# Kernel tuning notes

Measured on AMD Instinct MI355X. Metric: run time of the kernel, lower is better.

Reference implementation:

```python
import jax, jax.numpy as jnp
import numpy as np

EPS = 1e-5
B, C, H, W = 64, 256, 64, 64


def _masked_mean(p9, r0, r1, c0, c1):
    # p9: [B,3,3,9,H,W]; r0,r1: [B,3] int row bounds (per i); c0,c1: [B,3] int col bounds (per j)
    Hh, Ww = p9.shape[-2], p9.shape[-1]
    rows = jnp.arange(Hh, dtype=jnp.int32)
    cols = jnp.arange(Ww, dtype=jnp.int32)
    mr = (rows[None, None, :] >= r0[..., None]) & (rows[None, None, :] < r1[..., None])  # [B,3,H]
    mc = (cols[None, None, :] >= c0[..., None]) & (cols[None, None, :] < c1[..., None])  # [B,3,W]
    mask = (mr[:, :, None, :, None] & mc[:, None, :, None, :]).astype(p9.dtype)  # [B,3,3,H,W]
    cnt = mask.sum((-2, -1))  # [B,3,3]
    s = jnp.einsum('bijkhw,bijhw->bijk', p9, mask)
    return jnp.where(cnt[..., None] > 0, s / jnp.maximum(cnt, 1.0)[..., None], 0.0)  # [B,3,3,9]


def _subj_obj_bounds(bbox, Hh, Ww):
    # bbox: [B,4] = [y0,y1,x0,x1] normalized
    y0, y1, x0, x1 = bbox[:, 0], bbox[:, 1], bbox[:, 2], bbox[:, 3]
    ch = (y1 - y0) / 3.0
    cw = (x1 - x0) / 3.0
    idx = jnp.arange(3, dtype=bbox.dtype)
    r0 = jnp.floor(Hh * (y0[:, None] + idx * ch[:, None])).astype(jnp.int32)
    r1 = jnp.floor(Hh * (y0[:, None] + (idx + 1.0) * ch[:, None])).astype(jnp.int32)
    dr = r1 <= r0
    r1n = jnp.where(dr & (r1 < Hh - 1), r1 + 1, r1)
    r0n = jnp.where(dr & (r1 >= Hh - 1), r0 - 1, r0)
    c0 = jnp.floor(Ww * (x0[:, None] + idx * cw[:, None])).astype(jnp.int32)
    c1 = jnp.floor(Ww * (x0[:, None] + (idx + 1.0) * cw[:, None])).astype(jnp.int32)
    dc = c1 <= c0
    c1n = jnp.where(dc & (c1 < Ww), c1 + 1, c1)
    c0n = jnp.where(dc & (c1 >= Ww), c0 - 1, c0)
    return r0n, r1n, c0n, c1n


def _joint_bounds(bbox, bbox_s, bbox_o, Hh, Ww):
    # intersection of bbox with the 3x3 cells of union(bbox_s, bbox_o)
    uy0 = jnp.minimum(bbox_s[:, 0], bbox_o[:, 0])
    uy1 = jnp.maximum(bbox_s[:, 1], bbox_o[:, 1])
    ux0 = jnp.minimum(bbox_s[:, 2], bbox_o[:, 2])
    ux1 = jnp.maximum(bbox_s[:, 3], bbox_o[:, 3])
    ch = (uy1 - uy0) / 3.0
    cw = (ux1 - ux0) / 3.0
    idx = jnp.arange(3, dtype=bbox.dtype)
    ylo = uy0[:, None] + idx * ch[:, None]
    yhi = uy0[:, None] + (idx + 1.0) * ch[:, None]
    xlo = ux0[:, None] + idx * cw[:, None]
    xhi = ux0[:, None] + (idx + 1.0) * cw[:, None]
    r0 = jnp.floor(Hh * jnp.maximum(bbox[:, 0][:, None], ylo)).astype(jnp.int32)
    r1 = jnp.floor(Hh * jnp.minimum(bbox[:, 1][:, None], yhi)).astype(jnp.int32)
    c0 = jnp.floor(Ww * jnp.maximum(bbox[:, 2][:, None], xlo)).astype(jnp.int32)
    c1 = jnp.floor(Ww * jnp.minimum(bbox[:, 3][:, None], xhi)).astype(jnp.int32)
    return r0, r1, c0, c1


def setup_inputs() -> dict:
    key = jax.random.key(0)
    ks = jax.random.split(key, 16)
    feat = jax.random.normal(ks[0], (B, C, H, W), dtype=jnp.float32)

    def make_bbox(k):
        k1, k2, k3, k4 = jax.random.split(k, 4)
        y0 = jax.random.uniform(k1, (B,), minval=0.0, maxval=0.4)
        y1 = jnp.minimum(y0 + jax.random.uniform(k2, (B,), minval=0.3, maxval=0.55), 0.99)
        x0 = jax.random.uniform(k3, (B,), minval=0.0, maxval=0.4)
        x1 = jnp.minimum(x0 + jax.random.uniform(k4, (B,), minval=0.3, maxval=0.55), 0.99)
        return jnp.stack([y0, y1, x0, x1], axis=1).astype(jnp.float32)

    bbox_s = make_bbox(ks[1])
    bbox_o = make_bbox(ks[2])
    predicate = jax.random.uniform(ks[3], (B, 9), dtype=jnp.float32)
    conv_w = jax.random.normal(ks[4], (324, 256), dtype=jnp.float32) * 0.02
    conv_b = jax.random.normal(ks[5], (324,), dtype=jnp.float32) * 0.02
    bn2_g = jax.random.uniform(ks[6], (324,), minval=0.5, maxval=1.5)
    bn2_b = jax.random.normal(ks[7], (324,)) * 0.02
    bn2_m = jax.random.normal(ks[8], (324,)) * 0.02
    bn2_v = jax.random.uniform(ks[9], (324,), minval=0.5, maxval=1.5)
    fc1_w = jax.random.normal(ks[10], (40, 81), dtype=jnp.float32) * 0.1
    fc1_b = jnp.zeros((40,), jnp.float32)
    bn1_g = jax.random.uniform(ks[11], (40,), minval=0.5, maxval=1.5)
    bn1_b = jax.random.normal(ks[12], (40,)) * 0.02
    bn1_m = jax.random.normal(ks[13], (40,)) * 0.02
    bn1_v = jax.random.uniform(ks[14], (40,), minval=0.5, maxval=1.5)
    fc2_w = jax.random.normal(ks[15], (9, 40), dtype=jnp.float32) * 0.1
    fc2_b = jnp.zeros((9,), jnp.float32)
    return dict(feat=feat, bbox_s=bbox_s, bbox_o=bbox_o, predicate=predicate,
                conv_w=conv_w, conv_b=conv_b, bn2_g=bn2_g, bn2_b=bn2_b, bn2_m=bn2_m, bn2_v=bn2_v,
                fc1_w=fc1_w, fc1_b=fc1_b, bn1_g=bn1_g, bn1_b=bn1_b, bn1_m=bn1_m, bn1_v=bn1_v,
                fc2_w=fc2_w, fc2_b=fc2_b)


def reference(feat, bbox_s, bbox_o, predicate, conv_w, conv_b, bn2_g, bn2_b, bn2_m, bn2_v,
              fc1_w, fc1_b, bn1_g, bn1_b, bn1_m, bn1_v, fc2_w, fc2_b):
    # 1x1 conv 256 -> 324, then BatchNorm2d (inference mode)
    prs = jnp.einsum('bchw,oc->bohw', feat, conv_w) + conv_b[None, :, None, None]
    prs = (prs - bn2_m[None, :, None, None]) * (bn2_g / jnp.sqrt(bn2_v + EPS))[None, :, None, None] + bn2_b[None, :, None, None]
    Bb, _, Hh, Ww = prs.shape
    # channel layout: start = i*27 + j*9 + k  ->  reshape to [B,3,3,9,H,W]
    def bank(lo):
        return prs[:, lo:lo + 81].reshape(Bb, 3, 3, 9, Hh, Ww)
    prs_s, prs_o, prs_js, prs_jo = bank(0), bank(81), bank(162), bank(243)

    feature_s = _masked_mean(prs_s, *_subj_obj_bounds(bbox_s, Hh, Ww))
    feature_o = _masked_mean(prs_o, *_subj_obj_bounds(bbox_o, Hh, Ww))
    feature_j = (_masked_mean(prs_js, *_joint_bounds(bbox_s, bbox_s, bbox_o, Hh, Ww)) +
                 _masked_mean(prs_jo, *_joint_bounds(bbox_o, bbox_s, bbox_o, Hh, Ww)))

    f = feature_s + feature_o + feature_j            # [B,3,3,9]
    f = jnp.transpose(f, (0, 3, 1, 2)).reshape(Bb, 81)  # torch layout [B,9,3,3] flattened

    h = f @ fc1_w.T + fc1_b
    h = (h - bn1_m) * (bn1_g / jnp.sqrt(bn1_v + EPS)) + bn1_b
    logits = h @ fc2_w.T + fc2_b
    return jnp.sum(logits * predicate, axis=1)
```

## Files before the change

kernel.cpp:

```cpp
#include <hip/hip_runtime.h>
#include <hip/hip_bf16.h>
#include <cstdint>

#define BB 64
#define CC 256
#define HH 64
#define WW 64
#define EPSF 1e-5f

__device__ __forceinline__ void subj_bounds_dev(float y0, float y1, float x0, float x1,
                                                int* dst ) {
    float ch = __fdiv_rn(__fsub_rn(y1, y0), 3.0f);
    float cw = __fdiv_rn(__fsub_rn(x1, x0), 3.0f);
    for (int i = 0; i < 3; ++i) {
        float fi = (float)i;
        int R0 = (int)floorf(__fmul_rn((float)HH, __fadd_rn(y0, __fmul_rn(fi, ch))));
        int R1 = (int)floorf(__fmul_rn((float)HH, __fadd_rn(y0, __fmul_rn(__fadd_rn(fi, 1.0f), ch))));
        bool dr = (R1 <= R0);
        int R1n = (dr && (R1 < HH - 1)) ? R1 + 1 : R1;
        int R0n = (dr && (R1 >= HH - 1)) ? R0 - 1 : R0;
        int C0 = (int)floorf(__fmul_rn((float)WW, __fadd_rn(x0, __fmul_rn(fi, cw))));
        int C1 = (int)floorf(__fmul_rn((float)WW, __fadd_rn(x0, __fmul_rn(__fadd_rn(fi, 1.0f), cw))));
        bool dc = (C1 <= C0);
        int C1n = (dc && (C1 < WW)) ? C1 + 1 : C1;
        int C0n = (dc && (C1 >= WW)) ? C0 - 1 : C0;
        dst[i]     = R0n;
        dst[3 + i] = R1n;
        dst[6 + i] = C0n;
        dst[9 + i] = C1n;
    }
}

__device__ __forceinline__ void joint_bounds_dev(float uy0, float uy1, float ux0, float ux1,
                                                 float by0, float by1, float bx0, float bx1,
                                                 int* dst ) {
    float ch = __fdiv_rn(__fsub_rn(uy1, uy0), 3.0f);
    float cw = __fdiv_rn(__fsub_rn(ux1, ux0), 3.0f);
    for (int i = 0; i < 3; ++i) {
        float fi = (float)i;
        float ylo = __fadd_rn(uy0, __fmul_rn(fi, ch));
        float yhi = __fadd_rn(uy0, __fmul_rn(__fadd_rn(fi, 1.0f), ch));
        float xlo = __fadd_rn(ux0, __fmul_rn(fi, cw));
        float xhi = __fadd_rn(ux0, __fmul_rn(__fadd_rn(fi, 1.0f), cw));
        dst[i]     = (int)floorf(__fmul_rn((float)HH, fmaxf(by0, ylo)));
        dst[3 + i] = (int)floorf(__fmul_rn((float)HH, fminf(by1, yhi)));
        dst[6 + i] = (int)floorf(__fmul_rn((float)WW, fmaxf(bx0, xlo)));
        dst[9 + i] = (int)floorf(__fmul_rn((float)WW, fminf(bx1, xhi)));
    }
}

__global__ void k_bounds(const float* __restrict__ bbox_s,
                         const float* __restrict__ bbox_o,
                         int* __restrict__ bnds,
                         float* __restrict__ cntf) {
    int b = blockIdx.x * blockDim.x + threadIdx.x;
    if (b >= BB) return;
    float sy0 = bbox_s[b * 4 + 0], sy1 = bbox_s[b * 4 + 1];
    float sx0 = bbox_s[b * 4 + 2], sx1 = bbox_s[b * 4 + 3];
    float oy0 = bbox_o[b * 4 + 0], oy1 = bbox_o[b * 4 + 1];
    float ox0 = bbox_o[b * 4 + 2], ox1 = bbox_o[b * 4 + 3];

    int loc[4][12];
    subj_bounds_dev(sy0, sy1, sx0, sx1, loc[0]);
    subj_bounds_dev(oy0, oy1, ox0, ox1, loc[1]);
    float uy0 = fminf(sy0, oy0), uy1 = fmaxf(sy1, oy1);
    float ux0 = fminf(sx0, ox0), ux1 = fmaxf(sx1, ox1);
    joint_bounds_dev(uy0, uy1, ux0, ux1, sy0, sy1, sx0, sx1, loc[2]);
    joint_bounds_dev(uy0, uy1, ux0, ux1, oy0, oy1, ox0, ox1, loc[3]);

    int* ob = bnds + b * 48;
    float* oc = cntf + b * 36;
    for (int bank = 0; bank < 4; ++bank) {
        for (int q = 0; q < 12; ++q) ob[bank * 12 + q] = loc[bank][q];
        for (int i = 0; i < 3; ++i) {
            int rl = max(loc[bank][i], 0);
            int rh = min(loc[bank][3 + i], HH);
            int nrows = max(0, rh - rl);
            for (int j = 0; j < 3; ++j) {
                int cl = max(loc[bank][6 + j], 0);
                int chh = min(loc[bank][9 + j], WW);
                int ncols = max(0, chh - cl);
                oc[bank * 9 + i * 3 + j] = (float)(nrows * ncols);
            }
        }
    }
}

__global__ __launch_bounds__(64) void k_region_sums(const float* __restrict__ feat,
                                                    const int* __restrict__ bnds,
                                                    float* __restrict__ M) {
    int b = blockIdx.x >> 8;
    int c = blockIdx.x & 255;
    int l = threadIdx.x;

    __shared__ float S[64 * 65];

    const float4* src = (const float4*)(feat + ((size_t)(b * CC + c)) * (HH * WW));
    for (int it = 0; it < 16; ++it) {
        int f = it * 256 + l * 4;
        int h = f >> 6, w = f & 63;
        float4 v = src[it * 64 + l];
        float* dst = &S[h * 65 + w];
        dst[0] = v.x; dst[1] = v.y; dst[2] = v.z; dst[3] = v.w;
    }
    __syncthreads();

    {
        float run = 0.0f;
        int base = l * 65;
        for (int i = 0; i < 64; ++i) { run += S[base + i]; S[base + i] = run; }
    }
    __syncthreads();

    {
        float run = 0.0f;
        for (int i = 0; i < 64; ++i) { run += S[i * 65 + l]; S[i * 65 + l] = run; }
    }
    __syncthreads();

    if (l < 36) {
        const int* bk = bnds + b * 48 + (l / 9) * 12;
        int ij = l % 9, i = ij / 3, j = ij % 3;
        int r0 = bk[i], r1 = bk[3 + i], c0 = bk[6 + j], c1 = bk[9 + j];
        int rl = max(r0, 0), rh = min(r1, HH);
        int cl = max(c0, 0), chh = min(c1, WW);
        float s = 0.0f;
        if (rh > rl && chh > cl) {
            float a = S[(rh - 1) * 65 + (chh - 1)];
            float q = (cl > 0) ? S[(rh - 1) * 65 + (cl - 1)] : 0.0f;
            float p = (rl > 0) ? S[(rl - 1) * 65 + (chh - 1)] : 0.0f;
            float d = (rl > 0 && cl > 0) ? S[(rl - 1) * 65 + (cl - 1)] : 0.0f;
            s = a - q - p + d;
        }
        M[((size_t)(b * CC + c)) * 36 + l] = s;
    }
}

__global__ __launch_bounds__(384) void k_head(const float* __restrict__ M,
                                              const float* __restrict__ cntf,
                                              const float* __restrict__ conv_w,
                                              const float* __restrict__ conv_b,
                                              const float* __restrict__ g2,
                                              const float* __restrict__ b2,
                                              const float* __restrict__ m2,
                                              const float* __restrict__ v2,
                                              const float* __restrict__ fc1_w,
                                              const float* __restrict__ fc1_b,
                                              const float* __restrict__ g1,
                                              const float* __restrict__ b1,
                                              const float* __restrict__ m1,
                                              const float* __restrict__ v1,
                                              const float* __restrict__ fc2_w,
                                              const float* __restrict__ fc2_b,
                                              const float* __restrict__ pred,
                                              float* __restrict__ out) {
    int b = blockIdx.x;
    int t = threadIdx.x;

    __shared__ float Ml[256 * 37];
    __shared__ float val[324];
    __shared__ float fv[81];
    __shared__ float hv[40];
    __shared__ float lg[9];

    for (int i = t; i < 256 * 36; i += 384) {
        int c = i / 36, r = i - c * 36;
        Ml[c * 37 + r] = M[(size_t)b * (256 * 36) + i];
    }
    __syncthreads();

    if (t < 324) {
        int region = t / 9, k = t - region * 9;
        int bank = region / 9, ij = region - bank * 9;
        int ii = ij / 3, jj = ij % 3;
        int o = bank * 81 + ii * 27 + jj * 9 + k;
        float cnt = cntf[b * 36 + region];
        float v = 0.0f;
        if (cnt > 0.0f) {
            const float* w = conv_w + o * 256;
            float dot = 0.0f;
            #pragma unroll 8
            for (int c = 0; c < 256; ++c) dot += w[c] * Ml[c * 37 + region];
            float mean = dot / cnt;
            float sc = g2[o] / sqrtf(v2[o] + EPSF);
            v = (mean + conv_b[o] - m2[o]) * sc + b2[o];
        }
        val[region * 9 + k] = v;
    }
    __syncthreads();

    if (t < 81) {
        int k = t / 9, ij = t - k * 9;
        fv[t] = val[(0 + ij) * 9 + k] + val[(9 + ij) * 9 + k] +
                val[(18 + ij) * 9 + k] + val[(27 + ij) * 9 + k];
    }
    __syncthreads();

    if (t < 40) {
        float h = fc1_b[t];
        for (int u = 0; u < 81; ++u) h += fv[u] * fc1_w[t * 81 + u];
        h = (h - m1[t]) * (g1[t] / sqrtf(v1[t] + EPSF)) + b1[t];
        hv[t] = h;
    }
    __syncthreads();

    if (t < 9) {
        float lgt = fc2_b[t];
        for (int u = 0; u < 40; ++u) lgt += hv[u] * fc2_w[t * 40 + u];
        lg[t] = lgt * pred[b * 9 + t];
    }
    __syncthreads();

    if (t == 0) {
        float s = 0.0f;
        for (int i = 0; i < 9; ++i) s += lg[i];
        out[b] = s;
    }
}

extern "C" void kernel_launch(void* const* d_in, const int* in_sizes, int n_in,
                              void* d_out, int out_size, void* d_ws, size_t ws_size,
                              hipStream_t stream) {
    const float* feat   = (const float*)d_in[0];
    const float* bbox_s = (const float*)d_in[1];
    const float* bbox_o = (const float*)d_in[2];
    const float* pred   = (const float*)d_in[3];
    const float* conv_w = (const float*)d_in[4];
    const float* conv_b = (const float*)d_in[5];
    const float* g2     = (const float*)d_in[6];
    const float* b2     = (const float*)d_in[7];
    const float* m2     = (const float*)d_in[8];
    const float* v2     = (const float*)d_in[9];
    const float* fc1_w  = (const float*)d_in[10];
    const float* fc1_b  = (const float*)d_in[11];
    const float* g1     = (const float*)d_in[12];
    const float* b1     = (const float*)d_in[13];
    const float* m1     = (const float*)d_in[14];
    const float* v1     = (const float*)d_in[15];
    const float* fc2_w  = (const float*)d_in[16];
    const float* fc2_b  = (const float*)d_in[17];
    float* out = (float*)d_out;

    char* ws = (char*)d_ws;
    int*   bnds = (int*)ws;
    float* cntf = (float*)(ws + 12288);
    float* M    = (float*)(ws + 32768);

    k_bounds<<<1, 64, 0, stream>>>(bbox_s, bbox_o, bnds, cntf);
    k_region_sums<<<BB * CC, 64, 0, stream>>>(feat, bnds, M);
    k_head<<<BB, 384, 0, stream>>>(M, cntf, conv_w, conv_b, g2, b2, m2, v2,
                                   fc1_w, fc1_b, g1, b1, m1, v1, fc2_w, fc2_b,
                                   pred, out);
}
```

Before: 63.28 us.

## Fuse bounds into region-sum kernel and software-pipeline four planes per block

Drops the separate bounds kernel. Region bounds and counts are now recomputed inline, in the region-sum kernel and in the head, which removes one launch and a dependency. Each region-sum block now handles four channel planes and prefetches the next plane into registers while scanning the current one. This hides global load latency, at the cost of many more registers per thread and four times fewer blocks.

```diff
diff --git a/kernel.cpp b/kernel.cpp
--- a/kernel.cpp
+++ b/kernel.cpp
@@ -4,140 +4,149 @@
 
 #define BB 64
 #define CC 256
-#define HH 64
-#define WW 64
 #define EPSF 1e-5f
-
-__device__ __forceinline__ void subj_bounds_dev(float y0, float y1, float x0, float x1,
-                                                int* dst ) {
-    float ch = __fdiv_rn(__fsub_rn(y1, y0), 3.0f);
-    float cw = __fdiv_rn(__fsub_rn(x1, x0), 3.0f);
-    for (int i = 0; i < 3; ++i) {
-        float fi = (float)i;
-        int R0 = (int)floorf(__fmul_rn((float)HH, __fadd_rn(y0, __fmul_rn(fi, ch))));
-        int R1 = (int)floorf(__fmul_rn((float)HH, __fadd_rn(y0, __fmul_rn(__fadd_rn(fi, 1.0f), ch))));
+#define PLANES 4
+
+__device__ __forceinline__ void region_bounds(int bank, int i, int j,
+                                              float sy0, float sy1, float sx0, float sx1,
+                                              float oy0, float oy1, float ox0, float ox1,
+                                              int& r0, int& r1, int& c0, int& c1) {
+    float fi = (float)i, fj = (float)j;
+    if (bank < 2) {
+        float y0 = bank ? oy0 : sy0, y1 = bank ? oy1 : sy1;
+        float x0 = bank ? ox0 : sx0, x1 = bank ? ox1 : sx1;
+        float ch = __fdiv_rn(__fsub_rn(y1, y0), 3.0f);
+        float cw = __fdiv_rn(__fsub_rn(x1, x0), 3.0f);
+        int R0 = (int)floorf(__fmul_rn(64.0f, __fadd_rn(y0, __fmul_rn(fi, ch))));
+        int R1 = (int)floorf(__fmul_rn(64.0f, __fadd_rn(y0, __fmul_rn(__fadd_rn(fi, 1.0f), ch))));
         bool dr = (R1 <= R0);
-        int R1n = (dr && (R1 < HH - 1)) ? R1 + 1 : R1;
-        int R0n = (dr && (R1 >= HH - 1)) ? R0 - 1 : R0;
-        int C0 = (int)floorf(__fmul_rn((float)WW, __fadd_rn(x0, __fmul_rn(fi, cw))));
-        int C1 = (int)floorf(__fmul_rn((float)WW, __fadd_rn(x0, __fmul_rn(__fadd_rn(fi, 1.0f), cw))));
+        r1 = (dr && (R1 < 63)) ? R1 + 1 : R1;
+        r0 = (dr && (R1 >= 63)) ? R0 - 1 : R0;
+        int C0 = (int)floorf(__fmul_rn(64.0f, __fadd_rn(x0, __fmul_rn(fj, cw))));
+        int C1 = (int)floorf(__fmul_rn(64.0f, __fadd_rn(x0, __fmul_rn(__fadd_rn(fj, 1.0f), cw))));
         bool dc = (C1 <= C0);
-        int C1n = (dc && (C1 < WW)) ? C1 + 1 : C1;
-        int C0n = (dc && (C1 >= WW)) ? C0 - 1 : C0;
-        dst[i]     = R0n;
-        dst[3 + i] = R1n;
-        dst[6 + i] = C0n;
-        dst[9 + i] = C1n;
-    }
-}
-
-__device__ __forceinline__ void joint_bounds_dev(float uy0, float uy1, float ux0, float ux1,
-                                                 float by0, float by1, float bx0, float bx1,
-                                                 int* dst ) {
-    float ch = __fdiv_rn(__fsub_rn(uy1, uy0), 3.0f);
-    float cw = __fdiv_rn(__fsub_rn(ux1, ux0), 3.0f);
-    for (int i = 0; i < 3; ++i) {
-        float fi = (float)i;
+        c1 = (dc && (C1 < 64)) ? C1 + 1 : C1;
+        c0 = (dc && (C1 >= 64)) ? C0 - 1 : C0;
+    } else {
+        float by0 = (bank == 2) ? sy0 : oy0, by1 = (bank == 2) ? sy1 : oy1;
+        float bx0 = (bank == 2) ? sx0 : ox0, bx1 = (bank == 2) ? sx1 : ox1;
+        float uy0 = fminf(sy0, oy0), uy1 = fmaxf(sy1, oy1);
+        float ux0 = fminf(sx0, ox0), ux1 = fmaxf(sx1, ox1);
+        float ch = __fdiv_rn(__fsub_rn(uy1, uy0), 3.0f);
+        float cw = __fdiv_rn(__fsub_rn(ux1, ux0), 3.0f);
         float ylo = __fadd_rn(uy0, __fmul_rn(fi, ch));
         float yhi = __fadd_rn(uy0, __fmul_rn(__fadd_rn(fi, 1.0f), ch));
-        float xlo = __fadd_rn(ux0, __fmul_rn(fi, cw));
-        float xhi = __fadd_rn(ux0, __fmul_rn(__fadd_rn(fi, 1.0f), cw));
-        dst[i]     = (int)floorf(__fmul_rn((float)HH, fmaxf(by0, ylo)));
-        dst[3 + i] = (int)floorf(__fmul_rn((float)HH, fminf(by1, yhi)));
-        dst[6 + i] = (int)floorf(__fmul_rn((float)WW, fmaxf(bx0, xlo)));
-        dst[9 + i] = (int)floorf(__fmul_rn((float)WW, fminf(bx1, xhi)));
-    }
-}
-
-__global__ void k_bounds(const float* __restrict__ bbox_s,
-                         const float* __restrict__ bbox_o,
-                         int* __restrict__ bnds,
-                         float* __restrict__ cntf) {
-    int b = blockIdx.x * blockDim.x + threadIdx.x;
-    if (b >= BB) return;
+        float xlo = __fadd_rn(ux0, __fmul_rn(fj, cw));
+        float xhi = __fadd_rn(ux0, __fmul_rn(__fadd_rn(fj, 1.0f), cw));
+        r0 = (int)floorf(__fmul_rn(64.0f, fmaxf(by0, ylo)));
+        r1 = (int)floorf(__fmul_rn(64.0f, fminf(by1, yhi)));
+        c0 = (int)floorf(__fmul_rn(64.0f, fmaxf(bx0, xlo)));
+        c1 = (int)floorf(__fmul_rn(64.0f, fminf(bx1, xhi)));
+    }
+}
+
+__global__ __launch_bounds__(64) void k_region_sums(const float* __restrict__ feat,
+                                                    const float* __restrict__ bbox_s,
+                                                    const float* __restrict__ bbox_o,
+                                                    float* __restrict__ M) {
+    int blk = blockIdx.x;
+    int l = threadIdx.x;
+    int pid0 = blk * PLANES;
+    int b = pid0 >> 8;
+
     float sy0 = bbox_s[b * 4 + 0], sy1 = bbox_s[b * 4 + 1];
     float sx0 = bbox_s[b * 4 + 2], sx1 = bbox_s[b * 4 + 3];
     float oy0 = bbox_o[b * 4 + 0], oy1 = bbox_o[b * 4 + 1];
     float ox0 = bbox_o[b * 4 + 2], ox1 = bbox_o[b * 4 + 3];
 
-    int loc[4][12];
-    subj_bounds_dev(sy0, sy1, sx0, sx1, loc[0]);
-    subj_bounds_dev(oy0, oy1, ox0, ox1, loc[1]);
-    float uy0 = fminf(sy0, oy0), uy1 = fmaxf(sy1, oy1);
-    float ux0 = fminf(sx0, ox0), ux1 = fmaxf(sx1, ox1);
-    joint_bounds_dev(uy0, uy1, ux0, ux1, sy0, sy1, sx0, sx1, loc[2]);
-    joint_bounds_dev(uy0, uy1, ux0, ux1, oy0, oy1, ox0, ox1, loc[3]);
-
-    int* ob = bnds + b * 48;
-    float* oc = cntf + b * 36;
-    for (int bank = 0; bank < 4; ++bank) {
-        for (int q = 0; q < 12; ++q) ob[bank * 12 + q] = loc[bank][q];
-        for (int i = 0; i < 3; ++i) {
-            int rl = max(loc[bank][i], 0);
-            int rh = min(loc[bank][3 + i], HH);
-            int nrows = max(0, rh - rl);
-            for (int j = 0; j < 3; ++j) {
-                int cl = max(loc[bank][6 + j], 0);
-                int chh = min(loc[bank][9 + j], WW);
-                int ncols = max(0, chh - cl);
-                oc[bank * 9 + i * 3 + j] = (float)(nrows * ncols);
-            }
-        }
-    }
-}
-
-__global__ __launch_bounds__(64) void k_region_sums(const float* __restrict__ feat,
-                                                    const int* __restrict__ bnds,
-                                                    float* __restrict__ M) {
-    int b = blockIdx.x >> 8;
-    int c = blockIdx.x & 255;
-    int l = threadIdx.x;
+    int rl = 0, rh = 0, cl = 0, chh = 0;
+    if (l < 36) {
+        int bank = l / 9, ij = l % 9, i = ij / 3, j = ij % 3;
+        int r0, r1, c0, c1;
+        region_bounds(bank, i, j, sy0, sy1, sx0, sx1, oy0, oy1, ox0, ox1, r0, r1, c0, c1);
+        rl = max(r0, 0); rh = min(r1, 64);
+        cl = max(c0, 0); chh = min(c1, 64);
+    }
 
     __shared__ float S[64 * 65];
-
-    const float4* src = (const float4*)(feat + ((size_t)(b * CC + c)) * (HH * WW));
-    for (int it = 0; it < 16; ++it) {
-        int f = it * 256 + l * 4;
-        int h = f >> 6, w = f & 63;
-        float4 v = src[it * 64 + l];
-        float* dst = &S[h * 65 + w];
-        dst[0] = v.x; dst[1] = v.y; dst[2] = v.z; dst[3] = v.w;
-    }
-    __syncthreads();
-
-    {
-        float run = 0.0f;
-        int base = l * 65;
-        for (int i = 0; i < 64; ++i) { run += S[base + i]; S[base + i] = run; }
-    }
-    __syncthreads();
-
-    {
-        float run = 0.0f;
-        for (int i = 0; i < 64; ++i) { run += S[i * 65 + l]; S[i * 65 + l] = run; }
-    }
-    __syncthreads();
-
-    if (l < 36) {
-        const int* bk = bnds + b * 48 + (l / 9) * 12;
-        int ij = l % 9, i = ij / 3, j = ij % 3;
-        int r0 = bk[i], r1 = bk[3 + i], c0 = bk[6 + j], c1 = bk[9 + j];
-        int rl = max(r0, 0), rh = min(r1, HH);
-        int cl = max(c0, 0), chh = min(c1, WW);
-        float s = 0.0f;
-        if (rh > rl && chh > cl) {
-            float a = S[(rh - 1) * 65 + (chh - 1)];
-            float q = (cl > 0) ? S[(rh - 1) * 65 + (cl - 1)] : 0.0f;
-            float p = (rl > 0) ? S[(rl - 1) * 65 + (chh - 1)] : 0.0f;
-            float d = (rl > 0 && cl > 0) ? S[(rl - 1) * 65 + (cl - 1)] : 0.0f;
-            s = a - q - p + d;
-        }
-        M[((size_t)(b * CC + c)) * 36 + l] = s;
-    }
+    const float4* src = (const float4*)feat + (size_t)pid0 * 1024;
+
+    float4 ra[16], rb[16];
+
+#define LOADP(R, P)                                                         \
+    {                                                                       \
+        const float4* s2 = src + (size_t)(P) * 1024;                        \
+        _Pragma("unroll")                                                   \
+        for (int it = 0; it < 16; ++it) R[it] = s2[it * 64 + l];            \
+    }
+
+#define STOREP(R)                                                           \
+    {                                                                       \
+        _Pragma("unroll")                                                   \
+        for (int it = 0; it < 16; ++it) {                                   \
+            int f = it * 256 + l * 4;                                       \
+            int h = f >> 6, w = f & 63;                                     \
+            float* dst = &S[h * 65 + w];                                    \
+            dst[0] = R[it].x; dst[1] = R[it].y;                             \
+            dst[2] = R[it].z; dst[3] = R[it].w;                             \
+        }                                                                   \
+    }
+
+#define ROWSCAN()                                                           \
+    {                                                                       \
+        float run = 0.0f; int base = l * 65;                                \
+        _Pragma("unroll 16")                                                \
+        for (int i = 0; i < 64; ++i) { run += S[base + i]; S[base + i] = run; } \
+    }
+
+#define COLSCAN()                                                           \
+    {                                                                       \
+        float run = 0.0f;                                                   \
+        _Pragma("unroll 16")                                                \
+        for (int i = 0; i < 64; ++i) { run += S[i * 65 + l]; S[i * 65 + l] = run; } \
+    }
+
+#define EVALP(P)                                                            \
+    if (l < 36) {                                                           \
+        float s = 0.0f;                                                     \
+        if (rh > rl && chh > cl) {                                          \
+            float a2 = S[(rh - 1) * 65 + (chh - 1)];                        \
+            float q  = (cl > 0) ? S[(rh - 1) * 65 + (cl - 1)] : 0.0f;       \
+            float pp = (rl > 0) ? S[(rl - 1) * 65 + (chh - 1)] : 0.0f;      \
+            float dd = (rl > 0 && cl > 0) ? S[(rl - 1) * 65 + (cl - 1)] : 0.0f; \
+            s = a2 - q - pp + dd;                                           \
+        }                                                                   \
+        M[((size_t)(pid0 + (P))) * 36 + l] = s;                             \
+    }
+
+#define PLANE(CUR, NXT, P, PREFETCH)                                        \
+    __syncthreads();                                                        \
+    STOREP(CUR);                                                            \
+    __syncthreads();                                                        \
+    if (PREFETCH) LOADP(NXT, (P) + 1);                                      \
+    ROWSCAN();                                                              \
+    __syncthreads();                                                        \
+    COLSCAN();                                                              \
+    __syncthreads();                                                        \
+    EVALP(P);
+
+    LOADP(ra, 0);
+    PLANE(ra, rb, 0, 1);
+    PLANE(rb, ra, 1, 1);
+    PLANE(ra, rb, 2, 1);
+    PLANE(rb, ra, 3, 0);
+
+#undef LOADP
+#undef STOREP
+#undef ROWSCAN
+#undef COLSCAN
+#undef EVALP
+#undef PLANE
 }
 
 __global__ __launch_bounds__(384) void k_head(const float* __restrict__ M,
-                                              const float* __restrict__ cntf,
+                                              const float* __restrict__ bbox_s,
+                                              const float* __restrict__ bbox_o,
                                               const float* __restrict__ conv_w,
                                               const float* __restrict__ conv_b,
                                               const float* __restrict__ g2,
@@ -174,7 +183,17 @@
         int bank = region / 9, ij = region - bank * 9;
         int ii = ij / 3, jj = ij % 3;
         int o = bank * 81 + ii * 27 + jj * 9 + k;
-        float cnt = cntf[b * 36 + region];
+
+        float sy0 = bbox_s[b * 4 + 0], sy1 = bbox_s[b * 4 + 1];
+        float sx0 = bbox_s[b * 4 + 2], sx1 = bbox_s[b * 4 + 3];
+        float oy0 = bbox_o[b * 4 + 0], oy1 = bbox_o[b * 4 + 1];
+        float ox0 = bbox_o[b * 4 + 2], ox1 = bbox_o[b * 4 + 3];
+        int r0, r1, c0, c1;
+        region_bounds(bank, ii, jj, sy0, sy1, sx0, sx1, oy0, oy1, ox0, ox1, r0, r1, c0, c1);
+        int nrows = max(0, min(r1, 64) - max(r0, 0));
+        int ncols = max(0, min(c1, 64) - max(c0, 0));
+        float cnt = (float)(nrows * ncols);
+
         float v = 0.0f;
         if (cnt > 0.0f) {
             const float* w = conv_w + o * 256;
@@ -241,14 +260,10 @@
     const float* fc2_b  = (const float*)d_in[17];
     float* out = (float*)d_out;
 
-    char* ws = (char*)d_ws;
-    int*   bnds = (int*)ws;
-    float* cntf = (float*)(ws + 12288);
-    float* M    = (float*)(ws + 32768);
-
-    k_bounds<<<1, 64, 0, stream>>>(bbox_s, bbox_o, bnds, cntf);
-    k_region_sums<<<BB * CC, 64, 0, stream>>>(feat, bnds, M);
-    k_head<<<BB, 384, 0, stream>>>(M, cntf, conv_w, conv_b, g2, b2, m2, v2,
+    float* M = (float*)d_ws;
+
+    k_region_sums<<<(BB * CC) / PLANES, 64, 0, stream>>>(feat, bbox_s, bbox_o, M);
+    k_head<<<BB, 384, 0, stream>>>(M, bbox_s, bbox_o, conv_w, conv_b, g2, b2, m2, v2,
                                    fc1_w, fc1_b, g1, b1, m1, v1, fc2_w, fc2_b,
                                    pred, out);
 }
```

Result: slower. 65.06 us (+2.8%).
